# Kernel optimization log

Measured on AMD Instinct MI355X. Metric: run time of the kernel, lower is better.

Reference implementation:

```python
import jax, jax.numpy as jnp
import numpy as np

ALPHA = 3.0   # self.alpha
TAU = 0.1     # contrastive temperature
K = 8         # configs.k (top-k hyperedges per node)


def _scale(x, w, ehy, enod):
    """One scale of incidence_matrix_learn.
    x: [B, L, D] series tokens; w: [ws, D] word tokens;
    ehy: [H, D] hyperedge embedding table; enod: [N, D] node embedding table, N = L + ws.
    Returns (binary incidence matrix [N, H] float32, scalar contrastive loss).
    """
    B = x.shape[0]
    # concat_all[i]: cat(x.permute(0,2,1), word_expanded) -> [B, D, N]
    we = jnp.broadcast_to(w.T[None], (B,) + w.T.shape)          # [B, D, ws]
    concat = jnp.concatenate([jnp.transpose(x, (0, 2, 1)), we], axis=-1)  # [B, D, N]
    N, H = enod.shape[0], ehy.shape[0]
    # adjacency: softmax(relu(alpha * nodeec @ hyperen.T)) along hyperedge dim
    a = enod @ ehy.T                                            # [N, H]
    adj = jax.nn.softmax(jax.nn.relu(ALPHA * a), axis=-1)
    # top-k mask + threshold > 0.5 -> binary incidence matrix
    k = min(H, K)
    _, idx = jax.lax.top_k(adj, k)                              # [N, k]
    mask = jnp.zeros_like(adj).at[jnp.arange(N)[:, None], idx].set(1.0)
    adj_bin = ((adj * mask) > 0.5).astype(jnp.float32)          # [N, H]
    # positives: nodes sharing any hyperedge (build_pos_indices_from_edge_index),
    # equivalent to (A A^T > 0) with self excluded; dropping all-zero columns is a no-op here
    P = (adj_bin @ adj_bin.T > 0) & ~jnp.eye(N, dtype=bool)     # [N, N]
    cnt = P.sum(axis=1)                                         # positives per node
    # acl_loss_batched, vectorized over batch and nodes
    nodes = jnp.transpose(concat, (0, 2, 1))                    # [B, N, D]
    nrm = nodes / jnp.maximum(jnp.linalg.norm(nodes, axis=-1, keepdims=True), 1e-12)
    sim = jnp.einsum('bnd,bmd->bnm', nrm, nrm) / TAU            # [B, N, N]
    denom = jax.nn.logsumexp(sim, axis=-1)                      # [B, N]
    pos_mean = jnp.einsum('bnm,nm->bn', sim, P.astype(sim.dtype)) / jnp.maximum(cnt, 1)
    valid = cnt > 0                                             # [N]
    loss_sum = jnp.sum(jnp.where(valid[None, :], denom - pos_mean, 0.0))
    vc = B * valid.sum()
    loss = jnp.where(vc > 0, loss_sum / jnp.maximum(vc, 1), 0.0)
    return adj_bin, loss


def setup_inputs() -> dict:
    key = jax.random.key(0)
    ks = jax.random.split(key, 8)
    B, D = 64, 512
    return dict(
        x0=jax.random.normal(ks[0], (B, 512, D), dtype=jnp.float32),
        x1=jax.random.normal(ks[1], (B, 256, D), dtype=jnp.float32),
        word0=jax.random.normal(ks[2], (128, D), dtype=jnp.float32),
        word1=jax.random.normal(ks[3], (128, D), dtype=jnp.float32),
        embhy0=jax.random.normal(ks[4], (128, D), dtype=jnp.float32),
        embhy1=jax.random.normal(ks[5], (64, D), dtype=jnp.float32),
        embnod0=jax.random.normal(ks[6], (640, D), dtype=jnp.float32),
        embnod1=jax.random.normal(ks[7], (384, D), dtype=jnp.float32),
    )


def reference(x0, x1, word0, word1, embhy0, embhy1, embnod0, embnod1):
    a0, l0 = _scale(x0, word0, embhy0, embnod0)
    a1, l1 = _scale(x1, word1, embhy1, embnod1)
    return (a0, a1, l0 + l1)
```

## Files before the change

### kernel.cpp

```cpp
#include <hip/hip_runtime.h>


#define DDIM 512
#define BATCH 64
#define NGID 65536
#define NSLOT 6

typedef __attribute__((ext_vector_type(8))) short short8;
typedef __attribute__((ext_vector_type(4))) float f32x4;

__constant__ int CLS_SCALE[8] = {0, 0, 0, 1, 0, 1, 0, 1};
__constant__ int CLS_BU[8]    = {0, 1, 2, 0, 3, 1, 4, 2};
__constant__ int CLS_NTL[8]   = {5, 4, 3, 3, 2, 2, 1, 1};

__device__ __forceinline__ unsigned short f2bf(float f) {
  unsigned int u = __float_as_uint(f);
  u += 0x7fffu + ((u >> 16) & 1u);
  return (unsigned short)(u >> 16);
}

__device__ __forceinline__ void async16(const void* g, void* l) {
  __builtin_amdgcn_global_load_lds(
      (const __attribute__((address_space(1))) unsigned int*)g,
      (__attribute__((address_space(3))) unsigned int*)l, 16, 0, 0);
}

__device__ __forceinline__ int m3(int x) {
  x -= (x >= 6) ? 6 : 0;
  x -= (x >= 3) ? 3 : 0;
  return x;
}

__global__ __launch_bounds__(256) void prep_kernel(
    const float* __restrict__ enod0, const float* __restrict__ ehy0,
    const float* __restrict__ enod1, const float* __restrict__ ehy1,
    float* __restrict__ adj0, float* __restrict__ adj1,
    int* __restrict__ labels0, int* __restrict__ labels1,
    const float* __restrict__ x0, const float* __restrict__ w0,
    const float* __restrict__ x1, const float* __restrict__ w1,
    unsigned short* __restrict__ nhat0, unsigned short* __restrict__ nhat1,
    float* __restrict__ acc, int* __restrict__ ticket) {
  const int t = threadIdx.x;
  if (blockIdx.x < 1024) {
    if (blockIdx.x == 0 && t == 0) { acc[0] = 0.f; acc[1] = 0.f; ticket[0] = 0; }
    const bool s0 = blockIdx.x < 640;
    const int n = s0 ? blockIdx.x : blockIdx.x - 640;
    const int H = s0 ? 128 : 64;
    const float* enod = s0 ? enod0 : enod1;
    const float* ehy = s0 ? ehy0 : ehy1;
    float* out_adj = s0 ? adj0 : adj1;
    int* labels = s0 ? labels0 : labels1;
    __shared__ float erow[DDIM];
    __shared__ float red[128];
    __shared__ int lab;
    if (t < 128) ((float4*)erow)[t] = ((const float4*)(enod + (size_t)n * DDIM))[t];
    if (t == 0) lab = -1;
    __syncthreads();
    float v = 0.f;
    if (t < H) {
      const float4* hr = (const float4*)(ehy + (size_t)t * DDIM);
      float a = 0.f;
      #pragma unroll 8
      for (int d = 0; d < DDIM / 4; ++d) {
        float4 h = hr[d];
        float4 e = ((const float4*)erow)[d];
        a = fmaf(h.x, e.x, a); a = fmaf(h.y, e.y, a);
        a = fmaf(h.z, e.z, a); a = fmaf(h.w, e.w, a);
      }
      v = fmaxf(0.f, 3.0f * a);
    }
    if (t < 128) red[t] = v;
    __syncthreads();
    for (int s = 64; s > 0; s >>= 1) {
      if (t < s) red[t] = fmaxf(red[t], red[t + s]);
      __syncthreads();
    }
    const float mx = red[0];
    __syncthreads();
    const float e = (t < H) ? __expf(v - mx) : 0.f;
    if (t < 128) red[t] = e;
    __syncthreads();
    for (int s = 64; s > 0; s >>= 1) {
      if (t < s) red[t] += red[t + s];
      __syncthreads();
    }
    const float sum = red[0];
    if (t < H) {
      const float adj = e / sum;
      const float bin = (adj > 0.5f) ? 1.0f : 0.0f;
      out_adj[(size_t)n * H + t] = bin;
      if (bin > 0.f) lab = t;
    }
    __syncthreads();
    if (t == 0) labels[n] = lab;
  } else {
    const int wave = t >> 6;
    const int lane = t & 63;
    const int g = (blockIdx.x - 1024) * 4 + wave;
    const bool s0 = g < BATCH * 640;
    const int gg = s0 ? g : g - BATCH * 640;
    const int N = s0 ? 640 : 384;
    const int L = s0 ? 512 : 256;
    const float* x = s0 ? x0 : x1;
    const float* w = s0 ? w0 : w1;
    unsigned short* nhat = s0 ? nhat0 : nhat1;
    const int b = gg / N;
    const int n = gg - b * N;
    const float* src = (n < L) ? (x + ((size_t)b * L + n) * DDIM)
                               : (w + (size_t)(n - L) * DDIM);
    const float4* rowp = (const float4*)src;
    const float4 v0 = rowp[lane];
    const float4 v1 = rowp[lane + 64];
    float ss = v0.x * v0.x + v0.y * v0.y + v0.z * v0.z + v0.w * v0.w +
               v1.x * v1.x + v1.y * v1.y + v1.z * v1.z + v1.w * v1.w;
    #pragma unroll
    for (int off = 32; off > 0; off >>= 1) ss += __shfl_xor(ss, off);
    const float rinv = 1.0f / fmaxf(sqrtf(ss), 1e-12f);
    ushort4 o0, o1;
    o0.x = f2bf(v0.x * rinv); o0.y = f2bf(v0.y * rinv);
    o0.z = f2bf(v0.z * rinv); o0.w = f2bf(v0.w * rinv);
    o1.x = f2bf(v1.x * rinv); o1.y = f2bf(v1.y * rinv);
    o1.z = f2bf(v1.z * rinv); o1.w = f2bf(v1.w * rinv);
    ushort4* op = (ushort4*)(nhat + ((size_t)b * N + n) * DDIM);
    op[lane] = o0;
    op[lane + 64] = o1;
  }
}

__global__ __launch_bounds__(256) void cnt_kernel(
    const int* __restrict__ labels0, int* __restrict__ cnt0,
    const int* __restrict__ labels1, int* __restrict__ cnt1,
    int* __restrict__ valid) {
  const bool s0 = blockIdx.x == 0;
  const int* labels = s0 ? labels0 : labels1;
  int* cnt = s0 ? cnt0 : cnt1;
  int* validcnt = s0 ? valid : valid + 1;
  const int N = s0 ? 640 : 384;
  __shared__ int lab[640];
  __shared__ int hist[128];
  __shared__ int vc;
  const int t = threadIdx.x;
  if (t == 0) vc = 0;
  if (t < 128) hist[t] = 0;
  for (int i = t; i < N; i += 256) lab[i] = labels[i];
  __syncthreads();
  for (int i = t; i < N; i += 256)
    if (lab[i] >= 0) atomicAdd(&hist[lab[i]], 1);
  __syncthreads();
  int lv = 0;
  for (int i = t; i < N; i += 256) {
    const int c = (lab[i] >= 0) ? hist[lab[i]] - 1 : 0;
    cnt[i] = c;
    if (c > 0) ++lv;
  }
  if (lv > 0) atomicAdd(&vc, lv);
  __syncthreads();
  if (t == 0) *validcnt = vc;
}

__global__ __launch_bounds__(512, 4) void lse_kernel(
    const unsigned short* __restrict__ nhat0, const int* __restrict__ labels0,
    const unsigned short* __restrict__ nhat1, const int* __restrict__ labels1,
    float2* __restrict__ sp) {
  __shared__ short8 Bbuf[3][1024];
  __shared__ float2 redC[8][64];
  __shared__ int labS[640];
  const int tid = threadIdx.x;
  const int cls = blockIdx.x >> 7;
  const int half = (blockIdx.x >> 6) & 1;
  const int b = blockIdx.x & 63;
  const bool s0 = CLS_SCALE[cls] == 0;
  const int bu = CLS_BU[cls];
  const int ntl = CLS_NTL[cls];
  const int N = s0 ? 640 : 384;
  const unsigned short* nhat = s0 ? nhat0 : nhat1;
  const int* labels = s0 ? labels0 : labels1;
  const int gbase = s0 ? b * 640 : 40960 + b * 384;

  const int w = tid >> 6;
  const int lane = tid & 63;
  const int lrow = lane & 15;
  const int lq = lane >> 4;
  const int wq = w & 3;
  const int ut = 2 * bu + (w >> 2);

  for (int t = tid; t < N; t += 512) labS[t] = labels[t];

  const size_t base = (size_t)b * N * DDIM;
  const int bandrow0 = bu * 128;
  const int myrow = bandrow0 + w * 16 + lrow;
  const unsigned short* Ap = nhat + base + (size_t)myrow * DDIM + lq * 8;
  short8 a[16];
  #pragma unroll
  for (int ki = 0; ki < 16; ++ki) a[ki] = *(const short8*)(Ap + ki * 32);

  __syncthreads();

  int labn[4];
  #pragma unroll
  for (int r = 0; r < 4; ++r)
    labn[r] = labS[bandrow0 + w * 16 + lq * 4 + r];

  const int tv0 = 2 * bu + half;
  const unsigned short* Bp0 = nhat + base + (size_t)tv0 * 64 * DDIM;
  const int f0 = w * 2;
  #pragma unroll
  for (int pc = 0; pc < 2; ++pc) {
    #pragma unroll
    for (int fi = 0; fi < 2; ++fi) {
      const int f = f0 + fi, j = f >> 2, ks = f & 3;
      async16(Bp0 + (size_t)(j * 16 + lrow) * DDIM + pc * 128 + ks * 32 + lq * 8,
              &Bbuf[pc][f * 64]);
    }
  }

  float rSE[4] = {0.f, 0.f, 0.f, 0.f};
  float rPOS[4] = {0.f, 0.f, 0.f, 0.f};
  int slotb = 0;

  for (int ti = 0; ti < ntl; ++ti) {
    const int tv = tv0 + 2 * ti;
    const bool last = (ti == ntl - 1);
    const unsigned short* Bcur = nhat + base + (size_t)tv * 64 * DDIM;
    const unsigned short* Bnxt = Bcur + (size_t)128 * DDIM;
    const int sl[3] = {slotb, m3(slotb + 1), m3(slotb + 2)};

    f32x4 acc[4];
    #pragma unroll
    for (int j = 0; j < 4; ++j) acc[j] = (f32x4){0.f, 0.f, 0.f, 0.f};

    #pragma unroll
    for (int kc = 0; kc < 4; ++kc) {
      if (last && kc == 3) asm volatile("s_waitcnt vmcnt(0)" ::: "memory");
      else                 asm volatile("s_waitcnt vmcnt(2)" ::: "memory");
      __builtin_amdgcn_s_barrier();
      if (!(last && kc >= 2)) {
        const unsigned short* Bsrc = (kc < 2) ? Bcur : Bnxt;
        const int kcol = (kc + 2) & 3;
        short8* dst = &Bbuf[sl[(kc + 2) % 3]][0];
        #pragma unroll
        for (int fi = 0; fi < 2; ++fi) {
          const int f = f0 + fi, j = f >> 2, ks = f & 3;
          async16(Bsrc + (size_t)(j * 16 + lrow) * DDIM + kcol * 128 + ks * 32 + lq * 8,
                  dst + f * 64);
        }
      }
      const short8* bb = &Bbuf[sl[kc % 3]][0];
      #pragma unroll
      for (int ks = 0; ks < 4; ++ks) {
        const short8 b0 = bb[(0 * 4 + ks) * 64 + lane];
        const short8 b1 = bb[(1 * 4 + ks) * 64 + lane];
        const short8 b2 = bb[(2 * 4 + ks) * 64 + lane];
        const short8 b3 = bb[(3 * 4 + ks) * 64 + lane];
        const short8 av = a[kc * 4 + ks];
        acc[0] = __builtin_amdgcn_mfma_f32_16x16x32_bf16(av, b0, acc[0], 0, 0, 0);
        acc[1] = __builtin_amdgcn_mfma_f32_16x16x32_bf16(av, b1, acc[1], 0, 0, 0);
        acc[2] = __builtin_amdgcn_mfma_f32_16x16x32_bf16(av, b2, acc[2], 0, 0, 0);
        acc[3] = __builtin_amdgcn_mfma_f32_16x16x32_bf16(av, b3, acc[3], 0, 0, 0);
      }
    }

    const bool diag = (ut == tv);
    const bool colp = (tv >= 2 * bu + 2);
    float cSE[4] = {0.f, 0.f, 0.f, 0.f};
    float cPOS[4] = {0.f, 0.f, 0.f, 0.f};
    #pragma unroll
    for (int j = 0; j < 4; ++j) {
      const int v = tv * 64 + j * 16 + lrow;
      const int labm = labS[v];
      #pragma unroll
      for (int r = 0; r < 4; ++r) {
        const float sim = acc[j][r] * 10.0f;
        const float e = __expf(sim - 10.0f);
        rSE[r] += e;
        const bool match = (labn[r] >= 0) && (labm == labn[r]);
        const bool self = diag && (j == wq) && (lrow == lq * 4 + r);
        if (match && !self) rPOS[r] += sim;
        if (colp) {
          cSE[j] += e;
          if (match) cPOS[j] += sim;
        }
      }
    }
    if (colp) {
      #pragma unroll
      for (int off = 16; off <= 32; off <<= 1) {
        #pragma unroll
        for (int j = 0; j < 4; ++j) {
          cSE[j] += __shfl_xor(cSE[j], off);
          cPOS[j] += __shfl_xor(cPOS[j], off);
        }
      }
      if (lane < 16) {
        #pragma unroll
        for (int j = 0; j < 4; ++j) {
          float2 st; st.x = cSE[j]; st.y = cPOS[j];
          redC[w][j * 16 + lane] = st;
        }
      }
      asm volatile("s_waitcnt lgkmcnt(0)" ::: "memory");
      __builtin_amdgcn_s_barrier();
      if (tid < 64) {
        float se = 0.f, ps = 0.f;
        #pragma unroll
        for (int ww = 0; ww < 8; ++ww) {
          const float2 c = redC[ww][tid];
          se += c.x; ps += c.y;
        }
        float2 st; st.x = se; st.y = ps;
        sp[(size_t)(2 + bu) * NGID + gbase + tv * 64 + tid] = st;
      }
    }
    slotb = m3(slotb + 1);
  }

  #pragma unroll
  for (int off = 1; off <= 8; off <<= 1) {
    #pragma unroll
    for (int r = 0; r < 4; ++r) {
      rSE[r] += __shfl_xor(rSE[r], off);
      rPOS[r] += __shfl_xor(rPOS[r], off);
    }
  }
  if (lrow == 0) {
    #pragma unroll
    for (int r = 0; r < 4; ++r) {
      const int u = bandrow0 + w * 16 + lq * 4 + r;
      float2 st; st.x = rSE[r]; st.y = rPOS[r];
      sp[(size_t)half * NGID + gbase + u] = st;
    }
  }
}

__global__ __launch_bounds__(256) void loss_reduce(
    const float2* __restrict__ sp, const int* __restrict__ cnt0,
    const int* __restrict__ cnt1, float* __restrict__ acc,
    const int* __restrict__ valid, int* __restrict__ ticket,
    float* __restrict__ lossp) {
  __shared__ float r0[4], r1[4];
  const int t = threadIdx.x;
  float l0 = 0.f, l1 = 0.f;
  for (int g = blockIdx.x * 256 + t; g < NGID; g += 64 * 256) {
    const bool is0 = g < 40960;
    const int n = is0 ? (g % 640) : ((g - 40960) % 384);
    const int tt = n >> 6;
    const int nslots = 2 + (tt >> 1);
    float se = 0.f, pos = 0.f;
    for (int s = 0; s < nslots; ++s) {
      const float2 v = sp[(size_t)s * NGID + g];
      se += v.x; pos += v.y;
    }
    const int c = is0 ? cnt0[n] : cnt1[n];
    if (c > 0) {
      const float v = (10.0f + logf(se)) - pos / (float)c;
      if (is0) l0 += v; else l1 += v;
    }
  }
  #pragma unroll
  for (int off = 32; off > 0; off >>= 1) {
    l0 += __shfl_xor(l0, off);
    l1 += __shfl_xor(l1, off);
  }
  if ((t & 63) == 0) { r0[t >> 6] = l0; r1[t >> 6] = l1; }
  __syncthreads();
  if (t == 0) {
    atomicAdd(&acc[0], r0[0] + r0[1] + r0[2] + r0[3]);
    atomicAdd(&acc[1], r1[0] + r1[1] + r1[2] + r1[3]);
    __threadfence();
    const int done = atomicAdd(ticket, 1);
    if (done == 63) {
      const float a0v = atomicAdd(&acc[0], 0.0f);
      const float a1v = atomicAdd(&acc[1], 0.0f);
      float l = 0.f;
      if (valid[0] > 0) l += a0v / (float)(BATCH * valid[0]);
      if (valid[1] > 0) l += a1v / (float)(BATCH * valid[1]);
      lossp[0] = l;
    }
  }
}

extern "C" void kernel_launch(void* const* d_in, const int* in_sizes, int n_in,
                              void* d_out, int out_size, void* d_ws,
                              size_t ws_size, hipStream_t stream) {
  const float* x0 = (const float*)d_in[0];
  const float* x1 = (const float*)d_in[1];
  const float* w0 = (const float*)d_in[2];
  const float* w1 = (const float*)d_in[3];
  const float* ehy0 = (const float*)d_in[4];
  const float* ehy1 = (const float*)d_in[5];
  const float* enod0 = (const float*)d_in[6];
  const float* enod1 = (const float*)d_in[7];

  float* out = (float*)d_out;
  float* adj0 = out;
  float* adj1 = out + 640 * 128;
  float* lossp = out + 640 * 128 + 384 * 64;

  unsigned short* nhat0 = (unsigned short*)d_ws;
  unsigned short* nhat1 = nhat0 + (size_t)BATCH * 640 * DDIM;
  int* ip = (int*)(nhat1 + (size_t)BATCH * 384 * DDIM);
  int* labels0 = ip;
  int* labels1 = labels0 + 640;
  int* cnt0 = labels1 + 384;
  int* cnt1 = cnt0 + 640;
  int* valid = cnt1 + 384;
  int* ticket = valid + 2;
  float* acc = (float*)(ticket + 1);
  float2* sp = (float2*)((((size_t)(acc + 2)) + 255) & ~(size_t)255);

  prep_kernel<<<1024 + 16384, 256, 0, stream>>>(
      enod0, ehy0, enod1, ehy1, adj0, adj1, labels0, labels1,
      x0, w0, x1, w1, nhat0, nhat1, acc, ticket);
  cnt_kernel<<<2, 256, 0, stream>>>(labels0, cnt0, labels1, cnt1, valid);
  lse_kernel<<<1024, 512, 0, stream>>>(nhat0, labels0, nhat1, labels1, sp);
  loss_reduce<<<64, 256, 0, stream>>>(sp, cnt0, cnt1, acc, valid, ticket,
                                      lossp);
}
```

Baseline: 245.1 us.

## Restructure similarity kernel into symmetric 128x128 tile pairs with double-buffered A/B

Replaces the band-based lse kernel, which held A rows in registers and streamed B tiles through a triple buffer, with one block per upper-triangular 128x128 tile pair per batch. Each block stages both A and B in LDS with double buffering, computes a 4x4 MFMA register tile per wave, and emits both row and column partial sums for off-diagonal pairs. The aim is more reuse per loaded tile and better load balance across 1344 smaller blocks. In exchange it uses more accumulator registers and changes the slot layout that loss_reduce reads.

Result: faster. 235.0 us (-4.1%).

```diff
diff --git a/kernel.cpp b/kernel.cpp
--- a/kernel.cpp
+++ b/kernel.cpp
@@ -4,14 +4,14 @@
 #define DDIM 512
 #define BATCH 64
 #define NGID 65536
-#define NSLOT 6
+#define NSLOT 5
 
 typedef __attribute__((ext_vector_type(8))) short short8;
 typedef __attribute__((ext_vector_type(4))) float f32x4;
 
-__constant__ int CLS_SCALE[8] = {0, 0, 0, 1, 0, 1, 0, 1};
-__constant__ int CLS_BU[8]    = {0, 1, 2, 0, 3, 1, 4, 2};
-__constant__ int CLS_NTL[8]   = {5, 4, 3, 3, 2, 2, 1, 1};
+__constant__ int PAIR_SCALE[21] = {0,0,0,0,0,0,0,0,0,0,0,0,0,0,0, 1,1,1,1,1,1};
+__constant__ int PAIR_TU[21]    = {0,0,0,0,0,1,1,1,1,2,2,2,3,3,4, 0,0,0,1,1,2};
+__constant__ int PAIR_TV[21]    = {0,1,2,3,4,1,2,3,4,2,3,4,3,4,4, 0,1,2,1,2,2};
 
 __device__ __forceinline__ unsigned short f2bf(float f) {
   unsigned int u = __float_as_uint(f);
@@ -23,12 +23,6 @@
   __builtin_amdgcn_global_load_lds(
       (const __attribute__((address_space(1))) unsigned int*)g,
       (__attribute__((address_space(3))) unsigned int*)l, 16, 0, 0);
-}
-
-__device__ __forceinline__ int m3(int x) {
-  x -= (x >= 6) ? 6 : 0;
-  x -= (x >= 3) ? 3 : 0;
-  return x;
 }
 
 __global__ __launch_bounds__(256) void prep_kernel(
@@ -158,176 +152,162 @@
   if (t == 0) *validcnt = vc;
 }
 
-__global__ __launch_bounds__(512, 4) void lse_kernel(
+__global__ __launch_bounds__(256) void lse_kernel(
     const unsigned short* __restrict__ nhat0, const int* __restrict__ labels0,
     const unsigned short* __restrict__ nhat1, const int* __restrict__ labels1,
     float2* __restrict__ sp) {
-  __shared__ short8 Bbuf[3][1024];
-  __shared__ float2 redC[8][64];
-  __shared__ int labS[640];
+  __shared__ short8 Abuf[2][1024];
+  __shared__ short8 Bbuf[2][1024];
+  __shared__ int labU[128], labV[128];
+  __shared__ float2 rowBuf[128][2];
+  __shared__ float2 colBuf[128][2];
+
   const int tid = threadIdx.x;
-  const int cls = blockIdx.x >> 7;
-  const int half = (blockIdx.x >> 6) & 1;
+  const int p = blockIdx.x >> 6;
   const int b = blockIdx.x & 63;
-  const bool s0 = CLS_SCALE[cls] == 0;
-  const int bu = CLS_BU[cls];
-  const int ntl = CLS_NTL[cls];
+  const bool s0 = PAIR_SCALE[p] == 0;
+  const int tu = PAIR_TU[p], tv = PAIR_TV[p];
+  const bool diag = (tu == tv);
   const int N = s0 ? 640 : 384;
   const unsigned short* nhat = s0 ? nhat0 : nhat1;
   const int* labels = s0 ? labels0 : labels1;
   const int gbase = s0 ? b * 640 : 40960 + b * 384;
-
-  const int w = tid >> 6;
-  const int lane = tid & 63;
-  const int lrow = lane & 15;
-  const int lq = lane >> 4;
-  const int wq = w & 3;
-  const int ut = 2 * bu + (w >> 2);
-
-  for (int t = tid; t < N; t += 512) labS[t] = labels[t];
-
   const size_t base = (size_t)b * N * DDIM;
-  const int bandrow0 = bu * 128;
-  const int myrow = bandrow0 + w * 16 + lrow;
-  const unsigned short* Ap = nhat + base + (size_t)myrow * DDIM + lq * 8;
-  short8 a[16];
-  #pragma unroll
-  for (int ki = 0; ki < 16; ++ki) a[ki] = *(const short8*)(Ap + ki * 32);
-
-  __syncthreads();
-
-  int labn[4];
-  #pragma unroll
-  for (int r = 0; r < 4; ++r)
-    labn[r] = labS[bandrow0 + w * 16 + lq * 4 + r];
-
-  const int tv0 = 2 * bu + half;
-  const unsigned short* Bp0 = nhat + base + (size_t)tv0 * 64 * DDIM;
-  const int f0 = w * 2;
-  #pragma unroll
-  for (int pc = 0; pc < 2; ++pc) {
-    #pragma unroll
-    for (int fi = 0; fi < 2; ++fi) {
-      const int f = f0 + fi, j = f >> 2, ks = f & 3;
-      async16(Bp0 + (size_t)(j * 16 + lrow) * DDIM + pc * 128 + ks * 32 + lq * 8,
-              &Bbuf[pc][f * 64]);
-    }
-  }
-
-  float rSE[4] = {0.f, 0.f, 0.f, 0.f};
-  float rPOS[4] = {0.f, 0.f, 0.f, 0.f};
-  int slotb = 0;
-
-  for (int ti = 0; ti < ntl; ++ti) {
-    const int tv = tv0 + 2 * ti;
-    const bool last = (ti == ntl - 1);
-    const unsigned short* Bcur = nhat + base + (size_t)tv * 64 * DDIM;
-    const unsigned short* Bnxt = Bcur + (size_t)128 * DDIM;
-    const int sl[3] = {slotb, m3(slotb + 1), m3(slotb + 2)};
-
-    f32x4 acc[4];
-    #pragma unroll
-    for (int j = 0; j < 4; ++j) acc[j] = (f32x4){0.f, 0.f, 0.f, 0.f};
-
-    #pragma unroll
-    for (int kc = 0; kc < 4; ++kc) {
-      if (last && kc == 3) asm volatile("s_waitcnt vmcnt(0)" ::: "memory");
-      else                 asm volatile("s_waitcnt vmcnt(2)" ::: "memory");
-      __builtin_amdgcn_s_barrier();
-      if (!(last && kc >= 2)) {
-        const unsigned short* Bsrc = (kc < 2) ? Bcur : Bnxt;
-        const int kcol = (kc + 2) & 3;
-        short8* dst = &Bbuf[sl[(kc + 2) % 3]][0];
+
+  const int w = tid >> 6, lane = tid & 63;
+  const int wr = w >> 1, wc = w & 1;
+  const int lrow = lane & 15, lq = lane >> 4;
+
+  if (tid < 128) labU[tid] = labels[tu * 128 + tid];
+  else labV[tid - 128] = labels[tv * 128 + (tid - 128)];
+
+  const unsigned short* Asrc = nhat + base + (size_t)tu * 128 * DDIM;
+  const unsigned short* Bsrc = nhat + base + (size_t)tv * 128 * DDIM;
+
+  #define STAGE(buf, kk)                                                     \
+    do {                                                                     \
+      _Pragma("unroll")                                                      \
+      for (int i = 0; i < 4; ++i) {                                          \
+        const int f = i * 4 + w;                                             \
+        const int rg = f >> 1, ks = f & 1;                                   \
+        const size_t so = (size_t)(rg * 16 + lrow) * DDIM +                  \
+                          (kk) * 64 + ks * 32 + lq * 8;                      \
+        async16(Asrc + so, &Abuf[buf][f * 64]);                              \
+        async16(Bsrc + so, &Bbuf[buf][f * 64]);                              \
+      }                                                                      \
+    } while (0)
+
+  f32x4 acc[4][4];
+  #pragma unroll
+  for (int mi = 0; mi < 4; ++mi)
+    #pragma unroll
+    for (int ni = 0; ni < 4; ++ni) acc[mi][ni] = (f32x4){0.f, 0.f, 0.f, 0.f};
+
+  STAGE(0, 0);
+  __syncthreads();
+
+  for (int k = 0; k < 8; ++k) {
+    const int cur = k & 1;
+    if (k < 7) STAGE(cur ^ 1, k + 1);
+    #pragma unroll
+    for (int ks = 0; ks < 2; ++ks) {
+      short8 am[4], bn[4];
+      #pragma unroll
+      for (int mi = 0; mi < 4; ++mi)
+        am[mi] = Abuf[cur][((wr * 4 + mi) * 2 + ks) * 64 + lane];
+      #pragma unroll
+      for (int ni = 0; ni < 4; ++ni)
+        bn[ni] = Bbuf[cur][((wc * 4 + ni) * 2 + ks) * 64 + lane];
+      #pragma unroll
+      for (int mi = 0; mi < 4; ++mi)
         #pragma unroll
-        for (int fi = 0; fi < 2; ++fi) {
-          const int f = f0 + fi, j = f >> 2, ks = f & 3;
-          async16(Bsrc + (size_t)(j * 16 + lrow) * DDIM + kcol * 128 + ks * 32 + lq * 8,
-                  dst + f * 64);
+        for (int ni = 0; ni < 4; ++ni)
+          acc[mi][ni] = __builtin_amdgcn_mfma_f32_16x16x32_bf16(
+              am[mi], bn[ni], acc[mi][ni], 0, 0, 0);
+    }
+    __syncthreads();
+  }
+  #undef STAGE
+
+  float rSE[4][4], rPOS[4][4];
+  float cSE[4] = {0.f, 0.f, 0.f, 0.f};
+  float cPOS[4] = {0.f, 0.f, 0.f, 0.f};
+  int labn[4][4], labm[4];
+  #pragma unroll
+  for (int mi = 0; mi < 4; ++mi)
+    #pragma unroll
+    for (int r = 0; r < 4; ++r) {
+      rSE[mi][r] = 0.f; rPOS[mi][r] = 0.f;
+      labn[mi][r] = labU[wr * 64 + mi * 16 + lq * 4 + r];
+    }
+  #pragma unroll
+  for (int ni = 0; ni < 4; ++ni) labm[ni] = labV[wc * 64 + ni * 16 + lrow];
+
+  #pragma unroll
+  for (int mi = 0; mi < 4; ++mi) {
+    const int u_loc = wr * 64 + mi * 16 + lq * 4;
+    #pragma unroll
+    for (int ni = 0; ni < 4; ++ni) {
+      const int v_loc = wc * 64 + ni * 16 + lrow;
+      #pragma unroll
+      for (int r = 0; r < 4; ++r) {
+        const float sim = acc[mi][ni][r] * 10.0f;
+        const float e = __expf(sim - 10.0f);
+        rSE[mi][r] += e;
+        const bool match = (labn[mi][r] >= 0) && (labm[ni] == labn[mi][r]);
+        const bool self = diag && (u_loc + r == v_loc);
+        if (match && !self) rPOS[mi][r] += sim;
+        if (!diag) {
+          cSE[ni] += e;
+          if (match) cPOS[ni] += sim;
         }
       }
-      const short8* bb = &Bbuf[sl[kc % 3]][0];
-      #pragma unroll
-      for (int ks = 0; ks < 4; ++ks) {
-        const short8 b0 = bb[(0 * 4 + ks) * 64 + lane];
-        const short8 b1 = bb[(1 * 4 + ks) * 64 + lane];
-        const short8 b2 = bb[(2 * 4 + ks) * 64 + lane];
-        const short8 b3 = bb[(3 * 4 + ks) * 64 + lane];
-        const short8 av = a[kc * 4 + ks];
-        acc[0] = __builtin_amdgcn_mfma_f32_16x16x32_bf16(av, b0, acc[0], 0, 0, 0);
-        acc[1] = __builtin_amdgcn_mfma_f32_16x16x32_bf16(av, b1, acc[1], 0, 0, 0);
-        acc[2] = __builtin_amdgcn_mfma_f32_16x16x32_bf16(av, b2, acc[2], 0, 0, 0);
-        acc[3] = __builtin_amdgcn_mfma_f32_16x16x32_bf16(av, b3, acc[3], 0, 0, 0);
-      }
-    }
-
-    const bool diag = (ut == tv);
-    const bool colp = (tv >= 2 * bu + 2);
-    float cSE[4] = {0.f, 0.f, 0.f, 0.f};
-    float cPOS[4] = {0.f, 0.f, 0.f, 0.f};
-    #pragma unroll
-    for (int j = 0; j < 4; ++j) {
-      const int v = tv * 64 + j * 16 + lrow;
-      const int labm = labS[v];
+    }
+  }
+
+  #pragma unroll
+  for (int off = 1; off <= 8; off <<= 1)
+    #pragma unroll
+    for (int mi = 0; mi < 4; ++mi)
       #pragma unroll
       for (int r = 0; r < 4; ++r) {
-        const float sim = acc[j][r] * 10.0f;
-        const float e = __expf(sim - 10.0f);
-        rSE[r] += e;
-        const bool match = (labn[r] >= 0) && (labm == labn[r]);
-        const bool self = diag && (j == wq) && (lrow == lq * 4 + r);
-        if (match && !self) rPOS[r] += sim;
-        if (colp) {
-          cSE[j] += e;
-          if (match) cPOS[j] += sim;
-        }
-      }
-    }
-    if (colp) {
-      #pragma unroll
-      for (int off = 16; off <= 32; off <<= 1) {
-        #pragma unroll
-        for (int j = 0; j < 4; ++j) {
-          cSE[j] += __shfl_xor(cSE[j], off);
-          cPOS[j] += __shfl_xor(cPOS[j], off);
-        }
-      }
-      if (lane < 16) {
-        #pragma unroll
-        for (int j = 0; j < 4; ++j) {
-          float2 st; st.x = cSE[j]; st.y = cPOS[j];
-          redC[w][j * 16 + lane] = st;
-        }
-      }
-      asm volatile("s_waitcnt lgkmcnt(0)" ::: "memory");
-      __builtin_amdgcn_s_barrier();
-      if (tid < 64) {
-        float se = 0.f, ps = 0.f;
-        #pragma unroll
-        for (int ww = 0; ww < 8; ++ww) {
-          const float2 c = redC[ww][tid];
-          se += c.x; ps += c.y;
-        }
-        float2 st; st.x = se; st.y = ps;
-        sp[(size_t)(2 + bu) * NGID + gbase + tv * 64 + tid] = st;
-      }
-    }
-    slotb = m3(slotb + 1);
-  }
-
-  #pragma unroll
-  for (int off = 1; off <= 8; off <<= 1) {
-    #pragma unroll
-    for (int r = 0; r < 4; ++r) {
-      rSE[r] += __shfl_xor(rSE[r], off);
-      rPOS[r] += __shfl_xor(rPOS[r], off);
-    }
-  }
+        rSE[mi][r] += __shfl_xor(rSE[mi][r], off);
+        rPOS[mi][r] += __shfl_xor(rPOS[mi][r], off);
+      }
   if (lrow == 0) {
     #pragma unroll
-    for (int r = 0; r < 4; ++r) {
-      const int u = bandrow0 + w * 16 + lq * 4 + r;
-      float2 st; st.x = rSE[r]; st.y = rPOS[r];
-      sp[(size_t)half * NGID + gbase + u] = st;
+    for (int mi = 0; mi < 4; ++mi)
+      #pragma unroll
+      for (int r = 0; r < 4; ++r) {
+        float2 st; st.x = rSE[mi][r]; st.y = rPOS[mi][r];
+        rowBuf[wr * 64 + mi * 16 + lq * 4 + r][wc] = st;
+      }
+  }
+  if (!diag) {
+    #pragma unroll
+    for (int off = 16; off <= 32; off <<= 1)
+      #pragma unroll
+      for (int ni = 0; ni < 4; ++ni) {
+        cSE[ni] += __shfl_xor(cSE[ni], off);
+        cPOS[ni] += __shfl_xor(cPOS[ni], off);
+      }
+    if (lane < 16) {
+      #pragma unroll
+      for (int ni = 0; ni < 4; ++ni) {
+        float2 st; st.x = cSE[ni]; st.y = cPOS[ni];
+        colBuf[wc * 64 + ni * 16 + lrow][wr] = st;
+      }
+    }
+  }
+  __syncthreads();
+  if (tid < 128) {
+    const float2 ra = rowBuf[tid][0], rb = rowBuf[tid][1];
+    float2 st; st.x = ra.x + rb.x; st.y = ra.y + rb.y;
+    sp[(size_t)tv * NGID + gbase + tu * 128 + tid] = st;
+    if (!diag) {
+      const float2 ca = colBuf[tid][0], cb = colBuf[tid][1];
+      float2 ct; ct.x = ca.x + cb.x; ct.y = ca.y + cb.y;
+      sp[(size_t)tu * NGID + gbase + tv * 128 + tid] = ct;
     }
   }
 }
@@ -343,8 +323,7 @@
   for (int g = blockIdx.x * 256 + t; g < NGID; g += 64 * 256) {
     const bool is0 = g < 40960;
     const int n = is0 ? (g % 640) : ((g - 40960) % 384);
-    const int tt = n >> 6;
-    const int nslots = 2 + (tt >> 1);
+    const int nslots = is0 ? 5 : 3;
     float se = 0.f, pos = 0.f;
     for (int s = 0; s < nslots; ++s) {
       const float2 v = sp[(size_t)s * NGID + g];
@@ -412,7 +391,7 @@
       enod0, ehy0, enod1, ehy1, adj0, adj1, labels0, labels1,
       x0, w0, x1, w1, nhat0, nhat1, acc, ticket);
   cnt_kernel<<<2, 256, 0, stream>>>(labels0, cnt0, labels1, cnt1, valid);
-  lse_kernel<<<1024, 512, 0, stream>>>(nhat0, labels0, nhat1, labels1, sp);
+  lse_kernel<<<1344, 256, 0, stream>>>(nhat0, labels0, nhat1, labels1, sp);
   loss_reduce<<<64, 256, 0, stream>>>(sp, cnt0, cnt1, acc, valid, ticket,
                                       lossp);
 }
```
